# Kernel optimization log

Measured on AMD Instinct MI355X. Metric: run time of the kernel, lower is better.

The kernel has to match this reference:

```python
import jax, jax.numpy as jnp
import numpy as np

B, T, C = 2, 2048, 2048
N_HEAD = 16
HS = C // N_HEAD
D_LATENT = C // 2


def setup_inputs() -> dict:
    key = jax.random.key(0)
    ks = jax.random.split(key, 7)
    s = 0.02
    return {
        "x": jax.random.normal(ks[0], (B, T, C), dtype=jnp.float32),
        "Wq": jax.random.normal(ks[1], (C, C), dtype=jnp.float32) * s,
        "Wc": jax.random.normal(ks[2], (C, D_LATENT), dtype=jnp.float32) * s,
        "Wk": jax.random.normal(ks[3], (D_LATENT, C), dtype=jnp.float32) * s,
        "Wv": jax.random.normal(ks[4], (D_LATENT, C), dtype=jnp.float32) * s,
        "Wo": jax.random.normal(ks[5], (C, C), dtype=jnp.float32) * s,
        "bo": jnp.zeros((C,), dtype=jnp.float32),
    }


def reference(x, Wq, Wc, Wk, Wv, Wo, bo):
    b, t, c = x.shape
    # projections (torch Linear without bias, weights stored as (in, out))
    q = x @ Wq                    # (B,T,C)
    c_latent = x @ Wc             # (B,T,d_latent)
    k = c_latent @ Wk             # (B,T,C)
    v = c_latent @ Wv             # (B,T,C)
    # split heads -> (B,H,T,hs)
    q = q.reshape(b, t, N_HEAD, HS).transpose(0, 2, 1, 3)
    k = k.reshape(b, t, N_HEAD, HS).transpose(0, 2, 1, 3)
    v = v.reshape(b, t, N_HEAD, HS).transpose(0, 2, 1, 3)
    scale = 1.0 / jnp.sqrt(jnp.asarray(HS, dtype=x.dtype))
    scores = jnp.einsum('bhqd,bhkd->bhqk', q, k) * scale
    causal = jnp.tril(jnp.ones((t, t), dtype=bool))
    scores = jnp.where(causal, scores, jnp.finfo(scores.dtype).min)
    attn = jax.nn.softmax(scores, axis=-1)
    y = jnp.einsum('bhqk,bhkd->bhqd', attn, v)      # (B,H,T,hs)
    y = y.transpose(0, 2, 1, 3).reshape(b, t, c)
    return y @ Wo + bo
```

## Files before the change

kernel.cpp:

```cpp
#include <hip/hip_runtime.h>
#include <hip/hip_bf16.h>
#include <math.h>

typedef __hip_bfloat16 bf16;
typedef __attribute__((ext_vector_type(8))) short bf16x8;
typedef __attribute__((ext_vector_type(4))) float f32x4;

#define B_  2
#define T_  2048
#define C_  2048
#define H_  16
#define HS_ 128
#define DL_ 1024
#define M_  (B_ * T_)
#define NT64_ 32

__device__ inline void lds16(const bf16* g, bf16* l) {
    __builtin_amdgcn_global_load_lds(
        (const __attribute__((address_space(1))) void*)g,
        (__attribute__((address_space(3))) void*)l, 16, 0, 0);
}

__global__ __launch_bounds__(256) void cast_bf16_k(
    const float* __restrict__ in, bf16* __restrict__ out)
{
    const size_t i = ((size_t)blockIdx.x * 256 + threadIdx.x) * 8;
    const float4 a = *(const float4*)(in + i);
    const float4 b = *(const float4*)(in + i + 4);
    bf16 o[8];
    o[0] = __float2bfloat16(a.x); o[1] = __float2bfloat16(a.y);
    o[2] = __float2bfloat16(a.z); o[3] = __float2bfloat16(a.w);
    o[4] = __float2bfloat16(b.x); o[5] = __float2bfloat16(b.y);
    o[6] = __float2bfloat16(b.z); o[7] = __float2bfloat16(b.w);
    *(uint4*)(out + i) = *(const uint4*)o;
}

__global__ __launch_bounds__(256) void transpose_cast5(
    const float* __restrict__ s0, const float* __restrict__ s1,
    const float* __restrict__ s2, const float* __restrict__ s3,
    const float* __restrict__ s4,
    bf16* __restrict__ d0, bf16* __restrict__ d1, bf16* __restrict__ d2,
    bf16* __restrict__ d3, bf16* __restrict__ d4)
{
    const float* in; bf16* out; int R, Cc;
    switch (blockIdx.z) {
        case 0: in = s0; out = d0; R = C_;  Cc = C_;  break;
        case 1: in = s1; out = d1; R = C_;  Cc = DL_; break;
        case 2: in = s2; out = d2; R = DL_; Cc = C_;  break;
        case 3: in = s3; out = d3; R = DL_; Cc = C_;  break;
        default: in = s4; out = d4; R = C_; Cc = C_;  break;
    }
    const int bx = blockIdx.x * 32, by = blockIdx.y * 32;
    if (bx >= Cc || by >= R) return;
    __shared__ float t[32][33];
    const int tx = threadIdx.x & 31, ty = threadIdx.x >> 5;
#pragma unroll
    for (int i = 0; i < 32; i += 8)
        t[ty + i][tx] = in[(size_t)(by + ty + i) * Cc + bx + tx];
    __syncthreads();
#pragma unroll
    for (int i = 0; i < 32; i += 8)
        out[(size_t)(bx + ty + i) * R + by + tx] = __float2bfloat16(t[tx][ty + i]);
}

#define GEMM_CORE(A_, Bt_, Kdim)                                               \
    __shared__ __align__(16) bf16 As[128 * 64];                                \
    __shared__ __align__(16) bf16 Bs[128 * 64];                                \
    const int tid  = threadIdx.x;                                              \
    const int lane = tid & 63;                                                 \
    const int wave = tid >> 6;                                                 \
    const int wm = wave >> 1, wn = wave & 1;                                   \
    const int quad = lane >> 4, l16 = lane & 15;                               \
    const int sw8 = (l16 >> 1) & 7;                                            \
    f32x4 acc[4][4];                                                           \
    _Pragma("unroll")                                                          \
    for (int i = 0; i < 4; i++)                                                \
        _Pragma("unroll")                                                      \
        for (int j = 0; j < 4; j++) acc[i][j] = (f32x4){0.f, 0.f, 0.f, 0.f};   \
    const int srow = tid >> 3;                                                 \
    const int ssl  = (((tid & 7) ^ ((srow >> 1) & 7)) * 8);                    \
    const bf16* Ap = (A_)  + (size_t)(m0 + srow) * (Kdim) + ssl;               \
    const bf16* Bp = (Bt_) + (size_t)(n0 + srow) * (Kdim) + ssl;               \
    const size_t rstr = (size_t)32 * (Kdim);                                   \
    for (int k0 = 0; k0 < (Kdim); k0 += 64) {                                  \
        if (k0) __syncthreads();                                               \
        _Pragma("unroll")                                                      \
        for (int ii = 0; ii < 4; ii++) {                                       \
            lds16(Ap + ii * rstr + k0, As + ii * 2048 + tid * 8);              \
            lds16(Bp + ii * rstr + k0, Bs + ii * 2048 + tid * 8);              \
        }                                                                      \
        __syncthreads();                                                       \
        _Pragma("unroll")                                                      \
        for (int w = 0; w < 2; w++) {                                          \
            bf16x8 af[4], bfr[4];                                              \
            _Pragma("unroll")                                                  \
            for (int mi = 0; mi < 4; mi++)                                     \
                af[mi] = *(const bf16x8*)&As[(wm * 64 + mi * 16 + l16) * 64 +  \
                                            (((w << 2) | quad) ^ sw8) * 8];    \
            _Pragma("unroll")                                                  \
            for (int ni = 0; ni < 4; ni++)                                     \
                bfr[ni] = *(const bf16x8*)&Bs[(wn * 64 + ni * 16 + l16) * 64 + \
                                              (((w << 2) | quad) ^ sw8) * 8];  \
            _Pragma("unroll")                                                  \
            for (int mi = 0; mi < 4; mi++)                                     \
                _Pragma("unroll")                                              \
                for (int ni = 0; ni < 4; ni++)                                 \
                    acc[mi][ni] = __builtin_amdgcn_mfma_f32_16x16x32_bf16(     \
                        af[mi], bfr[ni], acc[mi][ni], 0, 0, 0);                \
        }                                                                      \
    }

__global__ __launch_bounds__(256) void gemm_bt_mfma(
    const bf16* __restrict__ A, const bf16* __restrict__ Bt,
    bf16* __restrict__ Cbf, float* __restrict__ Cf32,
    const float* __restrict__ bias, int M, int N, int K)
{
    const int m0 = blockIdx.y * 128, n0 = blockIdx.x * 128;
    GEMM_CORE(A, Bt, K)
#pragma unroll
    for (int mi = 0; mi < 4; mi++) {
#pragma unroll
        for (int ni = 0; ni < 4; ni++) {
            const int col = n0 + wn * 64 + ni * 16 + l16;
#pragma unroll
            for (int r = 0; r < 4; r++) {
                const int row = m0 + wm * 64 + mi * 16 + quad * 4 + r;
                if (Cf32)
                    Cf32[(size_t)row * N + col] = acc[mi][ni][r] + bias[col];
                else
                    Cbf[(size_t)row * N + col] = __float2bfloat16(acc[mi][ni][r]);
            }
        }
    }
}

__global__ __launch_bounds__(256) void gemm_qc_fused(
    const bf16* __restrict__ A, const bf16* __restrict__ Bt,
    bf16* __restrict__ Cq, bf16* __restrict__ Cc, int M, int K)
{
    const int m0 = blockIdx.y * 128, n0 = blockIdx.x * 128;
    GEMM_CORE(A, Bt, K)
    const bool is_q = (n0 < C_);
    const float scl = is_q ? 0.08838834764831845f : 1.0f;
    bf16* dst = is_q ? Cq : Cc;
    const int ld   = is_q ? C_ : DL_;
    const int coff = is_q ? 0 : C_;
#pragma unroll
    for (int mi = 0; mi < 4; mi++) {
#pragma unroll
        for (int ni = 0; ni < 4; ni++) {
            const int col = n0 - coff + wn * 64 + ni * 16 + l16;
#pragma unroll
            for (int r = 0; r < 4; r++) {
                const int row = m0 + wm * 64 + mi * 16 + quad * 4 + r;
                dst[(size_t)row * ld + col] = __float2bfloat16(acc[mi][ni][r] * scl);
            }
        }
    }
}

__global__ __launch_bounds__(256) void gemm_kv_fused(
    const bf16* __restrict__ clat, const bf16* __restrict__ Wk_t,
    const bf16* __restrict__ Wv_t, bf16* __restrict__ kk, bf16* __restrict__ vt)
{
    const int bid = blockIdx.x;
    const bf16 *A, *Bt; bf16* dst; int N, m0, n0;
    if (bid < 512) { A = clat; Bt = Wk_t; dst = kk; N = C_;
                     m0 = (bid >> 4) * 128; n0 = (bid & 15) * 128; }
    else           { const int t = bid - 512;
                     A = Wv_t; Bt = clat; dst = vt; N = M_;
                     m0 = (t >> 5) * 128; n0 = (t & 31) * 128; }
    GEMM_CORE(A, Bt, DL_)
#pragma unroll
    for (int mi = 0; mi < 4; mi++) {
#pragma unroll
        for (int ni = 0; ni < 4; ni++) {
            const int col = n0 + wn * 64 + ni * 16 + l16;
#pragma unroll
            for (int r = 0; r < 4; r++) {
                const int row = m0 + wm * 64 + mi * 16 + quad * 4 + r;
                dst[(size_t)row * N + col] = __float2bfloat16(acc[mi][ni][r]);
            }
        }
    }
}

__global__ __launch_bounds__(256, 2) void flash_dual(
    const bf16* __restrict__ Q, const bf16* __restrict__ K,
    const bf16* __restrict__ Vt, bf16* __restrict__ Y)
{
    __shared__ __align__(16) bf16 Ks[2][4][64][32];
    __shared__ __align__(16) bf16 Vs[2][2][128][32];
    __shared__ __align__(16) bf16 Ps[4][16][72];
    const int tid  = threadIdx.x;
    const int lane = tid & 63, wv = tid >> 6;
    const int quad = lane >> 4, l16 = lane & 15;
    const int sw = (l16 >> 1) & 3;
    const int bid = blockIdx.x;
    const int bh = (bid & 7) * 4 + ((bid >> 3) & 3);
    const int pa = bid >> 5;
    const int b = bh >> 4, h = bh & 15;
    const int qA0 = pa * 64, qB0 = (NT64_ - 1 - pa) * 64;
    const int jA = pa + 1;
    const int jB = NT64_ - pa;

    const int sr  = tid >> 2;
    const int ssl = ((tid & 3) ^ ((sr >> 1) & 3)) * 8;

    bf16x8 qfA[4], qfB[4];
    {
        const size_t rA = (size_t)(b * T_ + qA0 + wv * 16 + l16) * C_ + h * HS_;
        const size_t rB = (size_t)(b * T_ + qB0 + wv * 16 + l16) * C_ + h * HS_;
#pragma unroll
        for (int c = 0; c < 4; c++) {
            qfA[c] = *(const bf16x8*)(Q + rA + c * 32 + quad * 8);
            qfB[c] = *(const bf16x8*)(Q + rB + c * 32 + quad * 8);
        }
    }

    f32x4 oA[8], oB[8];
#pragma unroll
    for (int dt = 0; dt < 8; dt++) {
        oA[dt] = (f32x4){0.f, 0.f, 0.f, 0.f};
        oB[dt] = (f32x4){0.f, 0.f, 0.f, 0.f};
    }
    float lA[4] = {0.f, 0.f, 0.f, 0.f}, lB[4] = {0.f, 0.f, 0.f, 0.f};
    const int rbA = qA0 + wv * 16, rbB = qB0 + wv * 16;

    auto stage = [&](int j, int sbuf) {
        const int kv0 = j * 64;
#pragma unroll
        for (int kc = 0; kc < 4; kc++)
            lds16(K + (size_t)(b * T_ + kv0 + sr) * C_ + h * HS_ + kc * 32 + ssl,
                  &Ks[sbuf][kc][0][0] + tid * 8);
#pragma unroll
        for (int vc = 0; vc < 2; vc++)
#pragma unroll
            for (int hf = 0; hf < 2; hf++)
                lds16(Vt + (size_t)(h * HS_ + hf * 64 + sr) * M_ + b * T_ + kv0 + vc * 32 + ssl,
                      &Vs[sbuf][vc][hf * 64][0] + tid * 8);
    };

    auto sm_half = [&](const f32x4* s, int nt0, float* l_s, bool diag,
                       int kv0, int rowbase) {
        float p[2][4];
#pragma unroll
        for (int t = 0; t < 2; t++)
#pragma unroll
            for (int r = 0; r < 4; r++) {
                const int nt = nt0 + t;
                float e = __expf(s[nt][r]);
                if (diag) {
                    const int col = kv0 + nt * 16 + l16;
                    const int row = rowbase + quad * 4 + r;
                    if (col > row) e = 0.f;
                }
                p[t][r] = e;
            }
#pragma unroll
        for (int r = 0; r < 4; r++) l_s[r] += p[0][r] + p[1][r];
#pragma unroll
        for (int t = 0; t < 2; t++)
#pragma unroll
            for (int r = 0; r < 4; r++)
                Ps[wv][quad * 4 + r][(nt0 + t) * 16 + l16] = __float2bfloat16(p[t][r]);
        return *(const bf16x8*)&Ps[wv][l16][nt0 * 16 + quad * 8];
    };

    stage(0, 0);

    for (int j = 0; j < jA; j++) {
        const int kv0 = j * 64;
        stage(j + 1, (j + 1) & 1);
        __asm__ __volatile__("s_waitcnt vmcnt(8)" ::: "memory");
        __builtin_amdgcn_s_barrier();
        const int buf = j & 1;

        f32x4 sA[4], sB[4];
#pragma unroll
        for (int nt = 0; nt < 4; nt++) {
            sA[nt] = (f32x4){0.f, 0.f, 0.f, 0.f};
            sB[nt] = (f32x4){0.f, 0.f, 0.f, 0.f};
        }
        __builtin_amdgcn_s_setprio(1);
#pragma unroll
        for (int c = 0; c < 4; c++) {
            bf16x8 kf[4];
#pragma unroll
            for (int nt = 0; nt < 4; nt++)
                kf[nt] = *(const bf16x8*)&Ks[buf][c][nt * 16 + l16][(quad ^ sw) * 8];
#pragma unroll
            for (int nt = 0; nt < 4; nt++) {
                sB[nt] = __builtin_amdgcn_mfma_f32_16x16x32_bf16(qfB[c], kf[nt], sB[nt], 0, 0, 0);
                sA[nt] = __builtin_amdgcn_mfma_f32_16x16x32_bf16(qfA[c], kf[nt], sA[nt], 0, 0, 0);
            }
        }
        __builtin_amdgcn_s_setprio(0);

        const bool dA = (j == jA - 1);
        const bf16x8 pB0 = sm_half(sB, 0, lB, false, kv0, rbB);
        const bf16x8 pB1 = sm_half(sB, 2, lB, false, kv0, rbB);
        const bf16x8 pA0 = sm_half(sA, 0, lA, dA, kv0, rbA);
        const bf16x8 pA1 = sm_half(sA, 2, lA, dA, kv0, rbA);

        __builtin_amdgcn_s_setprio(1);
#pragma unroll
        for (int dt = 0; dt < 8; dt++) {
            const bf16x8 vf0 = *(const bf16x8*)&Vs[buf][0][dt * 16 + l16][(quad ^ sw) * 8];
            oB[dt] = __builtin_amdgcn_mfma_f32_16x16x32_bf16(pB0, vf0, oB[dt], 0, 0, 0);
            oA[dt] = __builtin_amdgcn_mfma_f32_16x16x32_bf16(pA0, vf0, oA[dt], 0, 0, 0);
        }
#pragma unroll
        for (int dt = 0; dt < 8; dt++) {
            const bf16x8 vf1 = *(const bf16x8*)&Vs[buf][1][dt * 16 + l16][(quad ^ sw) * 8];
            oB[dt] = __builtin_amdgcn_mfma_f32_16x16x32_bf16(pB1, vf1, oB[dt], 0, 0, 0);
            oA[dt] = __builtin_amdgcn_mfma_f32_16x16x32_bf16(pA1, vf1, oA[dt], 0, 0, 0);
        }
        __builtin_amdgcn_s_setprio(0);
        __asm__ __volatile__("s_waitcnt lgkmcnt(0)" ::: "memory");
        __builtin_amdgcn_s_barrier();
    }

    for (int j = jA; j < jB; j++) {
        const int kv0 = j * 64;
        if (j + 1 < jB) {
            stage(j + 1, (j + 1) & 1);
            __asm__ __volatile__("s_waitcnt vmcnt(8)" ::: "memory");
        } else {
            __asm__ __volatile__("s_waitcnt vmcnt(0)" ::: "memory");
        }
        __builtin_amdgcn_s_barrier();
        const int buf = j & 1;

        f32x4 sB[4];
#pragma unroll
        for (int nt = 0; nt < 4; nt++) sB[nt] = (f32x4){0.f, 0.f, 0.f, 0.f};
        __builtin_amdgcn_s_setprio(1);
#pragma unroll
        for (int c = 0; c < 4; c++) {
            bf16x8 kf[4];
#pragma unroll
            for (int nt = 0; nt < 4; nt++)
                kf[nt] = *(const bf16x8*)&Ks[buf][c][nt * 16 + l16][(quad ^ sw) * 8];
#pragma unroll
            for (int nt = 0; nt < 4; nt++)
                sB[nt] = __builtin_amdgcn_mfma_f32_16x16x32_bf16(qfB[c], kf[nt], sB[nt], 0, 0, 0);
        }
        __builtin_amdgcn_s_setprio(0);

        const bool dB = (j == jB - 1);
        const bf16x8 pB0 = sm_half(sB, 0, lB, dB, kv0, rbB);
        const bf16x8 pB1 = sm_half(sB, 2, lB, dB, kv0, rbB);

        __builtin_amdgcn_s_setprio(1);
#pragma unroll
        for (int dt = 0; dt < 8; dt++) {
            const bf16x8 vf0 = *(const bf16x8*)&Vs[buf][0][dt * 16 + l16][(quad ^ sw) * 8];
            oB[dt] = __builtin_amdgcn_mfma_f32_16x16x32_bf16(pB0, vf0, oB[dt], 0, 0, 0);
        }
#pragma unroll
        for (int dt = 0; dt < 8; dt++) {
            const bf16x8 vf1 = *(const bf16x8*)&Vs[buf][1][dt * 16 + l16][(quad ^ sw) * 8];
            oB[dt] = __builtin_amdgcn_mfma_f32_16x16x32_bf16(pB1, vf1, oB[dt], 0, 0, 0);
        }
        __builtin_amdgcn_s_setprio(0);
        __asm__ __volatile__("s_waitcnt lgkmcnt(0)" ::: "memory");
        __builtin_amdgcn_s_barrier();
    }

    auto finish = [&](int q0, f32x4* oacc, float* l_s) {
        float inv[4];
#pragma unroll
        for (int r = 0; r < 4; r++) {
            float l = l_s[r];
            l += __shfl_xor(l, 1);
            l += __shfl_xor(l, 2);
            l += __shfl_xor(l, 4);
            l += __shfl_xor(l, 8);
            inv[r] = 1.f / l;
        }
        const int rowbase = q0 + wv * 16;
#pragma unroll
        for (int dt = 0; dt < 8; dt++)
#pragma unroll
            for (int r = 0; r < 4; r++)
                Y[(size_t)(b * T_ + rowbase + quad * 4 + r) * C_ + h * HS_ + dt * 16 + l16] =
                    __float2bfloat16(oacc[dt][r] * inv[r]);
    };
    finish(qA0, oA, lA);
    finish(qB0, oB, lB);
}

extern "C" void kernel_launch(void* const* d_in, const int* in_sizes, int n_in,
                              void* d_out, int out_size, void* d_ws, size_t ws_size,
                              hipStream_t stream) {
    const float* x  = (const float*)d_in[0];
    const float* Wq = (const float*)d_in[1];
    const float* Wc = (const float*)d_in[2];
    const float* Wk = (const float*)d_in[3];
    const float* Wv = (const float*)d_in[4];
    const float* Wo = (const float*)d_in[5];
    const float* bo = (const float*)d_in[6];
    float* out = (float*)d_out;

    bf16* ws   = (bf16*)d_ws;
    bf16* x_bf = ws;
    bf16* Wq_t = x_bf + (size_t)M_ * C_;
    bf16* Wc_t = Wq_t + (size_t)C_ * C_;
    bf16* Wk_t = Wc_t + (size_t)DL_ * C_;
    bf16* Wv_t = Wk_t + (size_t)C_ * DL_;
    bf16* Wo_t = Wv_t + (size_t)C_ * DL_;
    bf16* q    = Wo_t + (size_t)C_ * C_;
    bf16* clat = q    + (size_t)M_ * C_;
    bf16* kk   = clat + (size_t)M_ * DL_;
    bf16* vt   = kk   + (size_t)M_ * C_;
    bf16* y    = vt   + (size_t)C_ * M_;

    const dim3 blk(256);

    cast_bf16_k<<<dim3((M_ * C_) / (256 * 8)), blk, 0, stream>>>(x, x_bf);
    transpose_cast5<<<dim3(C_ / 32, C_ / 32, 5), blk, 0, stream>>>(
        Wq, Wc, Wk, Wv, Wo, Wq_t, Wc_t, Wk_t, Wv_t, Wo_t);

    gemm_qc_fused<<<dim3((C_ + DL_) / 128, M_ / 128), blk, 0, stream>>>(
        x_bf, Wq_t, q, clat, M_, C_);
    gemm_kv_fused<<<dim3(1024), blk, 0, stream>>>(clat, Wk_t, Wv_t, kk, vt);

    flash_dual<<<dim3((NT64_ / 2) * H_ * B_), blk, 0, stream>>>(q, kk, vt, y);

    gemm_bt_mfma<<<dim3(C_ / 128, M_ / 128), blk, 0, stream>>>(
        y, Wo_t, nullptr, out, bo, M_, C_, C_);
}
```

Baseline: 357.0 us.

## Use 256x128 tiles with 512-thread blocks and triple-buffered async LDS pipeline

Replaces the single-buffered 128x128 GEMM core with a 256x128 tile computed by 8 waves (512 threads). Global-to-LDS loads now go through a three-stage ring buffer that prefetches two K-steps ahead, with manual vmcnt waits and raw barriers in place of __syncthreads. MFMA issue is wrapped in raised wave priority. The aim is to hide global load latency behind MFMA work and improve operand reuse per block, at the cost of much more LDS per block (144 KB) and fewer resident blocks.

After: 333.3 us. -6.6%, faster.

```diff
diff --git a/kernel.cpp b/kernel.cpp
--- a/kernel.cpp
+++ b/kernel.cpp
@@ -63,83 +63,90 @@
         out[(size_t)(bx + ty + i) * R + by + tx] = __float2bfloat16(t[tx][ty + i]);
 }
 
-#define GEMM_CORE(A_, Bt_, Kdim)                                               \
-    __shared__ __align__(16) bf16 As[128 * 64];                                \
-    __shared__ __align__(16) bf16 Bs[128 * 64];                                \
+#define GEMM250_CORE(A_, Bt_, ldA_, ldB_, Kdim_)                               \
+    __shared__ __align__(16) bf16 smem[3 * 24576];                 \
     const int tid  = threadIdx.x;                                              \
     const int lane = tid & 63;                                                 \
-    const int wave = tid >> 6;                                                 \
-    const int wm = wave >> 1, wn = wave & 1;                                   \
+    const int wid  = tid >> 6;                                       \
+    const int wr   = wid >> 1, wc = wid & 1;                    \
     const int quad = lane >> 4, l16 = lane & 15;                               \
-    const int sw8 = (l16 >> 1) & 7;                                            \
+    const int sw8  = (l16 >> 1) & 7;                                           \
     f32x4 acc[4][4];                                                           \
     _Pragma("unroll")                                                          \
     for (int i = 0; i < 4; i++)                                                \
         _Pragma("unroll")                                                      \
         for (int j = 0; j < 4; j++) acc[i][j] = (f32x4){0.f, 0.f, 0.f, 0.f};   \
-    const int srow = tid >> 3;                                                 \
-    const int ssl  = (((tid & 7) ^ ((srow >> 1) & 7)) * 8);                    \
-    const bf16* Ap = (A_)  + (size_t)(m0 + srow) * (Kdim) + ssl;               \
-    const bf16* Bp = (Bt_) + (size_t)(n0 + srow) * (Kdim) + ssl;               \
-    const size_t rstr = (size_t)32 * (Kdim);                                   \
-    for (int k0 = 0; k0 < (Kdim); k0 += 64) {                                  \
-        if (k0) __syncthreads();                                               \
+    const int sr  = tid >> 3;                                       \
+    const int ssl = ((tid & 7) ^ ((sr >> 1) & 7)) * 8;                         \
+    const bf16* pa = (A_)  + (size_t)(m0 + sr) * (ldA_) + ssl;                 \
+    const bf16* pb = (Bt_) + (size_t)(n0 + sr) * (ldB_) + ssl;                 \
+    const size_t a64 = (size_t)64 * (ldA_), b64 = (size_t)64 * (ldB_);         \
+    const int NT = (Kdim_) / 64;                                               \
+    _Pragma("unroll")                                                          \
+    for (int pt = 0; pt < 2; ++pt) {                  \
+        bf16* dst = smem + pt * 24576 + tid * 8;                               \
+        const size_t ko = (size_t)pt * 64;                                     \
+        lds16(pa + ko,           dst);                                         \
+        lds16(pa + a64 + ko,     dst + 4096);                                  \
+        lds16(pa + 2*a64 + ko,   dst + 8192);                                  \
+        lds16(pa + 3*a64 + ko,   dst + 12288);                                 \
+        lds16(pb + ko,           dst + 16384);                                 \
+        lds16(pb + b64 + ko,     dst + 20480);                                 \
+    }                                                                          \
+    int cur = 0, nxt2 = 2;                                                     \
+    for (int t = 0; t < NT; ++t) {                                             \
+        if (t == NT - 1) {                                                     \
+            __asm__ __volatile__("s_waitcnt vmcnt(0)" ::: "memory");           \
+        } else {                                                               \
+            __asm__ __volatile__("s_waitcnt vmcnt(6)" ::: "memory");           \
+        }                                                                      \
+        __builtin_amdgcn_s_barrier();                                          \
+        __builtin_amdgcn_sched_barrier(0);                                     \
+        if (t + 2 < NT) {                                                      \
+            bf16* dst = smem + nxt2 * 24576 + tid * 8;                         \
+            const size_t ko = (size_t)(t + 2) * 64;                            \
+            lds16(pa + ko,           dst);                                     \
+            lds16(pa + a64 + ko,     dst + 4096);                              \
+            lds16(pa + 2*a64 + ko,   dst + 8192);                              \
+            lds16(pa + 3*a64 + ko,   dst + 12288);                             \
+            lds16(pb + ko,           dst + 16384);                             \
+            lds16(pb + b64 + ko,     dst + 20480);                             \
+        }                                                                      \
+        const bf16* Ab = smem + cur * 24576;                                   \
+        const bf16* Bb = Ab + 16384;                                           \
+        bf16x8 af[4][2], bfr[4][2];                                            \
         _Pragma("unroll")                                                      \
-        for (int ii = 0; ii < 4; ii++) {                                       \
-            lds16(Ap + ii * rstr + k0, As + ii * 2048 + tid * 8);              \
-            lds16(Bp + ii * rstr + k0, Bs + ii * 2048 + tid * 8);              \
-        }                                                                      \
-        __syncthreads();                                                       \
+        for (int mi = 0; mi < 4; mi++)                                         \
+            _Pragma("unroll")                                                  \
+            for (int ks = 0; ks < 2; ks++)                                     \
+                af[mi][ks] = *(const bf16x8*)&Ab[(wr*64 + mi*16 + l16)*64 +    \
+                                                 (((ks<<2)|quad) ^ sw8)*8];    \
         _Pragma("unroll")                                                      \
-        for (int w = 0; w < 2; w++) {                                          \
-            bf16x8 af[4], bfr[4];                                              \
+        for (int ni = 0; ni < 4; ni++)                                         \
             _Pragma("unroll")                                                  \
-            for (int mi = 0; mi < 4; mi++)                                     \
-                af[mi] = *(const bf16x8*)&As[(wm * 64 + mi * 16 + l16) * 64 +  \
-                                            (((w << 2) | quad) ^ sw8) * 8];    \
-            _Pragma("unroll")                                                  \
-            for (int ni = 0; ni < 4; ni++)                                     \
-                bfr[ni] = *(const bf16x8*)&Bs[(wn * 64 + ni * 16 + l16) * 64 + \
-                                              (((w << 2) | quad) ^ sw8) * 8];  \
+            for (int ks = 0; ks < 2; ks++)                                     \
+                bfr[ni][ks] = *(const bf16x8*)&Bb[(wc*64 + ni*16 + l16)*64 +   \
+                                                  (((ks<<2)|quad) ^ sw8)*8];   \
+        __builtin_amdgcn_s_setprio(1);                                         \
+        _Pragma("unroll")                                                      \
+        for (int ks = 0; ks < 2; ks++)                                         \
             _Pragma("unroll")                                                  \
             for (int mi = 0; mi < 4; mi++)                                     \
                 _Pragma("unroll")                                              \
                 for (int ni = 0; ni < 4; ni++)                                 \
                     acc[mi][ni] = __builtin_amdgcn_mfma_f32_16x16x32_bf16(     \
-                        af[mi], bfr[ni], acc[mi][ni], 0, 0, 0);                \
-        }                                                                      \
-    }
-
-__global__ __launch_bounds__(256) void gemm_bt_mfma(
+                        af[mi][ks], bfr[ni][ks], acc[mi][ni], 0, 0, 0);        \
+        __builtin_amdgcn_s_setprio(0);                                         \
+        cur  = (cur  == 2) ? 0 : cur  + 1;                                     \
+        nxt2 = (nxt2 == 2) ? 0 : nxt2 + 1;                                     \
+    }
+
+__global__ __launch_bounds__(512, 2) void gemm_qc_250(
     const bf16* __restrict__ A, const bf16* __restrict__ Bt,
-    bf16* __restrict__ Cbf, float* __restrict__ Cf32,
-    const float* __restrict__ bias, int M, int N, int K)
-{
-    const int m0 = blockIdx.y * 128, n0 = blockIdx.x * 128;
-    GEMM_CORE(A, Bt, K)
-#pragma unroll
-    for (int mi = 0; mi < 4; mi++) {
-#pragma unroll
-        for (int ni = 0; ni < 4; ni++) {
-            const int col = n0 + wn * 64 + ni * 16 + l16;
-#pragma unroll
-            for (int r = 0; r < 4; r++) {
-                const int row = m0 + wm * 64 + mi * 16 + quad * 4 + r;
-                if (Cf32)
-                    Cf32[(size_t)row * N + col] = acc[mi][ni][r] + bias[col];
-                else
-                    Cbf[(size_t)row * N + col] = __float2bfloat16(acc[mi][ni][r]);
-            }
-        }
-    }
-}
-
-__global__ __launch_bounds__(256) void gemm_qc_fused(
-    const bf16* __restrict__ A, const bf16* __restrict__ Bt,
-    bf16* __restrict__ Cq, bf16* __restrict__ Cc, int M, int K)
-{
-    const int m0 = blockIdx.y * 128, n0 = blockIdx.x * 128;
-    GEMM_CORE(A, Bt, K)
+    bf16* __restrict__ Cq, bf16* __restrict__ Cc)
+{
+    const int m0 = blockIdx.y * 256, n0 = blockIdx.x * 128;
+    GEMM250_CORE(A, Bt, C_, C_, C_)
     const bool is_q = (n0 < C_);
     const float scl = is_q ? 0.08838834764831845f : 1.0f;
     bf16* dst = is_q ? Cq : Cc;
@@ -149,37 +156,57 @@
     for (int mi = 0; mi < 4; mi++) {
 #pragma unroll
         for (int ni = 0; ni < 4; ni++) {
-            const int col = n0 - coff + wn * 64 + ni * 16 + l16;
+            const int col = n0 - coff + wc * 64 + ni * 16 + l16;
 #pragma unroll
             for (int r = 0; r < 4; r++) {
-                const int row = m0 + wm * 64 + mi * 16 + quad * 4 + r;
+                const int row = m0 + wr * 64 + mi * 16 + quad * 4 + r;
                 dst[(size_t)row * ld + col] = __float2bfloat16(acc[mi][ni][r] * scl);
             }
         }
     }
 }
 
-__global__ __launch_bounds__(256) void gemm_kv_fused(
+__global__ __launch_bounds__(512, 2) void gemm_kv_250(
     const bf16* __restrict__ clat, const bf16* __restrict__ Wk_t,
     const bf16* __restrict__ Wv_t, bf16* __restrict__ kk, bf16* __restrict__ vt)
 {
     const int bid = blockIdx.x;
     const bf16 *A, *Bt; bf16* dst; int N, m0, n0;
-    if (bid < 512) { A = clat; Bt = Wk_t; dst = kk; N = C_;
-                     m0 = (bid >> 4) * 128; n0 = (bid & 15) * 128; }
-    else           { const int t = bid - 512;
+    if (bid < 256) { A = clat; Bt = Wk_t; dst = kk; N = C_;
+                     m0 = (bid >> 4) * 256; n0 = (bid & 15) * 128; }
+    else           { const int t2 = bid - 256;
                      A = Wv_t; Bt = clat; dst = vt; N = M_;
-                     m0 = (t >> 5) * 128; n0 = (t & 31) * 128; }
-    GEMM_CORE(A, Bt, DL_)
+                     m0 = (t2 >> 5) * 256; n0 = (t2 & 31) * 128; }
+    GEMM250_CORE(A, Bt, DL_, DL_, DL_)
 #pragma unroll
     for (int mi = 0; mi < 4; mi++) {
 #pragma unroll
         for (int ni = 0; ni < 4; ni++) {
-            const int col = n0 + wn * 64 + ni * 16 + l16;
+            const int col = n0 + wc * 64 + ni * 16 + l16;
 #pragma unroll
             for (int r = 0; r < 4; r++) {
-                const int row = m0 + wm * 64 + mi * 16 + quad * 4 + r;
+                const int row = m0 + wr * 64 + mi * 16 + quad * 4 + r;
                 dst[(size_t)row * N + col] = __float2bfloat16(acc[mi][ni][r]);
+            }
+        }
+    }
+}
+
+__global__ __launch_bounds__(512, 2) void gemm_out_250(
+    const bf16* __restrict__ A, const bf16* __restrict__ Bt,
+    float* __restrict__ Cf32, const float* __restrict__ bias)
+{
+    const int m0 = blockIdx.y * 256, n0 = blockIdx.x * 128;
+    GEMM250_CORE(A, Bt, C_, C_, C_)
+#pragma unroll
+    for (int mi = 0; mi < 4; mi++) {
+#pragma unroll
+        for (int ni = 0; ni < 4; ni++) {
+            const int col = n0 + wc * 64 + ni * 16 + l16;
+#pragma unroll
+            for (int r = 0; r < 4; r++) {
+                const int row = m0 + wr * 64 + mi * 16 + quad * 4 + r;
+                Cf32[(size_t)row * C_ + col] = acc[mi][ni][r] + bias[col];
             }
         }
     }
@@ -417,17 +444,18 @@
     bf16* y    = vt   + (size_t)C_ * M_;
 
     const dim3 blk(256);
+    const dim3 blk512(512);
 
     cast_bf16_k<<<dim3((M_ * C_) / (256 * 8)), blk, 0, stream>>>(x, x_bf);
     transpose_cast5<<<dim3(C_ / 32, C_ / 32, 5), blk, 0, stream>>>(
         Wq, Wc, Wk, Wv, Wo, Wq_t, Wc_t, Wk_t, Wv_t, Wo_t);
 
-    gemm_qc_fused<<<dim3((C_ + DL_) / 128, M_ / 128), blk, 0, stream>>>(
-        x_bf, Wq_t, q, clat, M_, C_);
-    gemm_kv_fused<<<dim3(1024), blk, 0, stream>>>(clat, Wk_t, Wv_t, kk, vt);
+    gemm_qc_250<<<dim3((C_ + DL_) / 128, M_ / 256), blk512, 0, stream>>>(
+        x_bf, Wq_t, q, clat);
+    gemm_kv_250<<<dim3(512), blk512, 0, stream>>>(clat, Wk_t, Wv_t, kk, vt);
 
     flash_dual<<<dim3((NT64_ / 2) * H_ * B_), blk, 0, stream>>>(q, kk, vt, y);
 
-    gemm_bt_mfma<<<dim3(C_ / 128, M_ / 128), blk, 0, stream>>>(
-        y, Wo_t, nullptr, out, bo, M_, C_, C_);
-}
+    gemm_out_250<<<dim3(C_ / 128, M_ / 256), blk512, 0, stream>>>(
+        y, Wo_t, out, bo);
+}
```
